# Kernel optimization log

Measured on AMD Instinct MI355X. Metric: run time of the kernel, lower is better.

## Reference

```python
import jax, jax.numpy as jnp
import numpy as np


def axisangle2mat(p):
    # p: [N, 6] = (rotation vector rx,ry,rz, translation tx,ty,tz) -> [N, 3, 4]
    v = p[:, :3]
    t = p[:, 3:]
    theta = jnp.sqrt(jnp.sum(v * v, axis=-1) + 1e-12)  # [N]
    k = v / theta[:, None]
    kx, ky, kz = k[:, 0], k[:, 1], k[:, 2]
    zero = jnp.zeros_like(kx)
    K = jnp.stack([
        jnp.stack([zero, -kz, ky], -1),
        jnp.stack([kz, zero, -kx], -1),
        jnp.stack([-ky, kx, zero], -1),
    ], -2)  # [N,3,3]
    I = jnp.eye(3, dtype=p.dtype)
    s = jnp.sin(theta)[:, None, None]
    c = (1.0 - jnp.cos(theta))[:, None, None]
    R = I + s * K + c * jnp.matmul(K, K)
    return jnp.concatenate([R, t[:, :, None]], axis=-1)  # [N,3,4]


def grid_sample_3d(vol, grid):
    # vol: [D,H,W]; grid: [...,3] with last dim (x,y,z) in [-1,1].
    # Replicates F.grid_sample(mode='bilinear', padding_mode='zeros', align_corners=False).
    D, H, W = vol.shape
    ix = ((grid[..., 0] + 1.0) * W - 1.0) * 0.5
    iy = ((grid[..., 1] + 1.0) * H - 1.0) * 0.5
    iz = ((grid[..., 2] + 1.0) * D - 1.0) * 0.5
    x0 = jnp.floor(ix); y0 = jnp.floor(iy); z0 = jnp.floor(iz)
    fx = ix - x0; fy = iy - y0; fz = iz - z0
    vol_flat = vol.reshape(-1)
    out = jnp.zeros(grid.shape[:-1], vol.dtype)
    for dz in (0, 1):
        for dy in (0, 1):
            for dx in (0, 1):
                xc = x0 + dx; yc = y0 + dy; zc = z0 + dz
                wgt = ((fx if dx else 1.0 - fx) * (fy if dy else 1.0 - fy) * (fz if dz else 1.0 - fz))
                valid = ((xc >= 0) & (xc < W) & (yc >= 0) & (yc < H) & (zc >= 0) & (zc < D))
                xi = jnp.clip(xc, 0, W - 1).astype(jnp.int32)
                yi = jnp.clip(yc, 0, H - 1).astype(jnp.int32)
                zi = jnp.clip(zc, 0, D - 1).astype(jnp.int32)
                v = vol_flat[(zi * H + yi) * W + xi]
                out = out + jnp.where(valid, v * wgt, 0.0)
    return out


def setup_inputs() -> dict:
    key = jax.random.key(0)
    ks = jax.random.split(key, 8)
    B, n, D, H, W = 4096, 2048, 256, 256, 256
    x = jax.random.normal(ks[0], (1, 1, D, H, W), dtype=jnp.float32)
    # voxel-space sample points inside the volume
    sampleGrid = jax.random.uniform(ks[1], (B, 3), dtype=jnp.float32) * jnp.array([W - 1, H - 1, D - 1], jnp.float32)
    ax = jnp.concatenate([
        jax.random.normal(ks[2], (B, 1, 3), dtype=jnp.float32) * 0.1,   # small rotations
        jax.random.normal(ks[3], (B, 1, 3), dtype=jnp.float32) * 5.0,   # translations (voxels)
    ], axis=-1)
    low = jax.random.uniform(ks[4], (B, 1, 3), dtype=jnp.float32) * 2.0
    ext = jax.random.uniform(ks[5], (B, 1, 3), dtype=jnp.float32) * 4.0 + 1.0
    bound = jnp.concatenate([low, low + ext], axis=1)  # [B,2,3], bound[:,1] > bound[:,0]
    A = jax.random.normal(ks[6], (B, 3, 3), dtype=jnp.float32) * 0.3
    InvCovScaled = jnp.einsum('bij,bkj->bik', A, A) + 0.5 * jnp.eye(3, dtype=jnp.float32)  # SPD
    xyz_psf = jax.random.normal(ks[7], (B, n, 3), dtype=jnp.float32)
    psf_sigma = jnp.ones((1,), jnp.float32)  # unused in forward (as in the original)
    return dict(x=x, sampleGrid=sampleGrid, ax=ax, bound=bound,
                InvCovScaled=InvCovScaled, psf_sigma=psf_sigma, xyz_psf=xyz_psf)


def reference(x, sampleGrid, ax, bound, InvCovScaled, psf_sigma, xyz_psf):
    # x: [1,1,D,H,W]; sampleGrid: [B,3]; ax: [B,1,6]; bound: [B,2,3];
    # InvCovScaled: [B,3,3]; xyz_psf: [B,n,3] (the torch.randn draw, made explicit)
    W = x.shape[-1]; H = x.shape[-2]; D = x.shape[-3]
    size = (W, H, D)  # matches torch: size = [x.shape[-1], x.shape[-2], x.shape[-3]]
    scaled_xyz_psf = 2.0 * jax.nn.sigmoid(xyz_psf) - 1.0                      # [B,n,3]
    half = (bound[:, 1, :] - bound[:, 0, :]) * 0.5                            # [B,3]
    bound_psf = scaled_xyz_psf * half[:, None]                                # [B,n,3]
    mat = axisangle2mat(ax.reshape(-1, 6)).reshape(ax.shape[:-1] + (3, 4))    # [B,1,3,4]
    R = mat[:, 0, :, :3]                                                      # [B,3,3]
    T = mat[:, 0, :, 3]                                                       # [B,3]
    # trans_first=True: R @ (p + T)
    mat_sampleGrid = jnp.einsum('bij,bj->bi', R, sampleGrid + T)[:, None]     # [B,1,3]
    psf_sampleGrid = mat_sampleGrid + bound_psf                               # [B,n,3]
    norm = jnp.array([size[0] - 1, size[1] - 1, size[2] - 1], psf_sampleGrid.dtype)
    grid = 2.0 * (psf_sampleGrid / norm - 0.5)
    psf_x = grid_sample_3d(x[0, 0], grid)                                     # [B,n]
    # Mahalanobis-style weights: exp(-0.5 * c^T InvCov c)
    q = jnp.einsum('bni,bij,bnj->bn', bound_psf, InvCovScaled, bound_psf)
    w = jnp.exp(-0.5 * q)                                                     # [B,n]
    y = jnp.sum(psf_x * w, axis=-1) / jnp.sum(w, axis=-1)                     # [B]
    return y
```

## Files before the change

### kernel.cpp

```cpp
#include <hip/hip_runtime.h>
#include <hip/hip_fp16.h>
#include <math.h>

constexpr int NT   = 256;
constexpr int WPB  = 4;
constexpr int DIMV = 256;
constexpr int RS   = 8;
constexpr int QROW = 9;
constexpr int QSLICE = RS * QROW;

__device__ __forceinline__ float rflf(float x) {
    return __uint_as_float(__builtin_amdgcn_readfirstlane(__float_as_uint(x)));
}
__device__ __forceinline__ float fexp2(float x) {
#if __has_builtin(__builtin_amdgcn_exp2f)
    return __builtin_amdgcn_exp2f(x);
#else
    return __expf(x * 0.6931471805599453f);
#endif
}
__device__ __forceinline__ float ffract(float x) {
#if __has_builtin(__builtin_amdgcn_fractf)
    return __builtin_amdgcn_fractf(x);
#else
    return x - floorf(x);
#endif
}
__device__ __forceinline__ unsigned pk16(float a, float b) {
    __half2 h = __float22half2_rn(make_float2(a, b));
    return __builtin_bit_cast(unsigned, h);
}
__device__ __forceinline__ __half2 u2h(unsigned u) {
    return __builtin_bit_cast(__half2, u);
}

__global__ __launch_bounds__(NT, 4) void psf_sample_kernel(
    const float* __restrict__ vol,
    const float* __restrict__ sampleGrid,
    const float* __restrict__ ax,
    const float* __restrict__ bound,
    const float* __restrict__ invcov,
    const float* __restrict__ xyz,
    float* __restrict__ out,
    int n, int B)
{
    const int tid  = threadIdx.x;
    const int wid  = tid >> 6;
    const int lane = tid & 63;
    const int b    = blockIdx.x * WPB + wid;
    const bool valid = b < B;

    __shared__ uint4 s_q[WPB][RS * QSLICE];

    const float LOG2E = 1.4426950408889634f;
    float cix = 0, ciy = 0, ciz = 0, hx = 0, hy = 0, hz = 0, addrC = 0;
    float Bxx = 0, Byy = 0, Bzz = 0, Bxy = 0, Bxz = 0, Byz = 0;
    bool fast = false;

    if (valid) {
        const float v0 = ax[b*6+0], v1 = ax[b*6+1], v2 = ax[b*6+2];
        const float t0 = ax[b*6+3], t1 = ax[b*6+4], t2 = ax[b*6+5];
        const float theta = sqrtf(v0*v0 + v1*v1 + v2*v2 + 1e-12f);
        const float inv = 1.0f / theta;
        const float kx = v0*inv, ky = v1*inv, kz = v2*inv;
        const float sn = __sinf(theta);
        const float cn = 1.0f - __cosf(theta);
        const float R00 = 1.0f - cn*(ky*ky + kz*kz);
        const float R01 = -sn*kz + cn*kx*ky;
        const float R02 =  sn*ky + cn*kx*kz;
        const float R10 =  sn*kz + cn*kx*ky;
        const float R11 = 1.0f - cn*(kx*kx + kz*kz);
        const float R12 = -sn*kx + cn*ky*kz;
        const float R20 = -sn*ky + cn*kx*kz;
        const float R21 =  sn*kx + cn*ky*kz;
        const float R22 = 1.0f - cn*(kx*kx + ky*ky);
        const float g0 = sampleGrid[b*3+0] + t0;
        const float g1 = sampleGrid[b*3+1] + t1;
        const float g2 = sampleGrid[b*3+2] + t2;
        const float ms0 = R00*g0 + R01*g1 + R02*g2;
        const float ms1 = R10*g0 + R11*g1 + R12*g2;
        const float ms2 = R20*g0 + R21*g1 + R22*g2;
        const float h0 = (bound[b*6+3] - bound[b*6+0]) * 0.5f;
        const float h1 = (bound[b*6+4] - bound[b*6+1]) * 0.5f;
        const float h2 = (bound[b*6+5] - bound[b*6+2]) * 0.5f;
        const float M00 = invcov[b*9+0], M01 = invcov[b*9+1], M02 = invcov[b*9+2];
        const float M11 = invcov[b*9+4], M12 = invcov[b*9+5], M22 = invcov[b*9+8];

        Bxx = rflf(-0.5f * M00 * h0 * h0 * LOG2E);
        Byy = rflf(-0.5f * M11 * h1 * h1 * LOG2E);
        Bzz = rflf(-0.5f * M22 * h2 * h2 * LOG2E);
        Bxy = rflf(-M01 * h0 * h1 * LOG2E);
        Bxz = rflf(-M02 * h0 * h2 * LOG2E);
        Byz = rflf(-M12 * h1 * h2 * LOG2E);

        const float kk = 256.0f / 255.0f;
        cix = rflf(fmaf(ms0, kk, -0.5f));
        ciy = rflf(fmaf(ms1, kk, -0.5f));
        ciz = rflf(fmaf(ms2, kk, -0.5f));
        hx  = rflf(h0 * kk);
        hy  = rflf(h1 * kk);
        hz  = rflf(h2 * kk);

        const int bx = __builtin_amdgcn_readfirstlane((int)floorf(cix - hx - 1e-3f));
        const int by = __builtin_amdgcn_readfirstlane((int)floorf(ciy - hy - 1e-3f));
        const int bz = __builtin_amdgcn_readfirstlane((int)floorf(ciz - hz - 1e-3f));
        addrC = rflf((float)(bz * QSLICE + by * QROW + bx));
        fast = (hx <= 2.9f) && (hy <= 2.9f) && (hz <= 2.9f);

        if (fast) {
            const int lx = lane & 7, ly = lane >> 3;
            float pv = 0.0f, pdx = 0.0f, pdy = 0.0f, pdxy = 0.0f;
            #pragma unroll
            for (int p = 0; p < RS; ++p) {
                const int gx = bx + lx, gy = by + ly, gz = bz + p;
                float v = 0.0f;
                if ((unsigned)gx < (unsigned)DIMV && (unsigned)gy < (unsigned)DIMV &&
                    (unsigned)gz < (unsigned)DIMV)
                    v = vol[((size_t)gz * DIMV + gy) * DIMV + gx];
                const float v10 = __shfl(v, (lane + 1) & 63);
                const float v01 = __shfl(v, (lane + 8) & 63);
                const float v11 = __shfl(v, (lane + 9) & 63);
                const float dx  = v10 - v;
                const float dy  = v01 - v;
                const float dxy = (v11 - v10) - dy;
                if (p > 0) {
                    s_q[wid][((p - 1) * RS + ly) * QROW + lx] =
                        make_uint4(pk16(pv, v), pk16(pdx, dx),
                                   pk16(pdy, dy), pk16(pdxy, dxy));
                }
                pv = v; pdx = dx; pdy = dy; pdxy = dxy;
            }
        }
    }
    __syncthreads();

    if (valid) {
        float sum_wx = 0.0f, sum_w = 0.0f;
        const uint4* __restrict__ sreg = s_q[wid];

        auto doSample = [&](float rx, float ry, float rz) {
            const float ex = fexp2(rx * -LOG2E);
            const float ey = fexp2(ry * -LOG2E);
            const float ez = fexp2(rz * -LOG2E);
            const float sx = (1.0f - ex) * __builtin_amdgcn_rcpf(1.0f + ex);
            const float sy = (1.0f - ey) * __builtin_amdgcn_rcpf(1.0f + ey);
            const float sz = (1.0f - ez) * __builtin_amdgcn_rcpf(1.0f + ez);

            const float ixf = fmaf(sx, hx, cix);
            const float iyf = fmaf(sy, hy, ciy);
            const float izf = fmaf(sz, hz, ciz);
            const float x0f = floorf(ixf), y0f = floorf(iyf), z0f = floorf(izf);
            const float fx = ffract(ixf), fy = ffract(iyf), fz = ffract(izf);

            float val;
            if (fast) {
                const float ef = fmaf(z0f, (float)QSLICE,
                                 fmaf(y0f, (float)QROW, x0f - addrC));
                const int e = (int)ef;
                const uint4 q = sreg[e];
                const __half2 v01  = u2h(q.x);
                const __half2 dx01 = u2h(q.y);
                const __half2 dy01 = u2h(q.z);
                const __half2 dxy01= u2h(q.w);
                const __half2 fx2  = __float2half2_rn(fx);
                const __half2 fy2  = __float2half2_rn(fy);
                const __half2 fxy2 = __hmul2(fx2, fy2);
                const __half2 acc  = __hfma2(fxy2, dxy01,
                                     __hfma2(fy2, dy01,
                                     __hfma2(fx2, dx01, v01)));
                const float a0 = __low2float(acc);
                const float a1 = __high2float(acc);
                val = fmaf(fz, a1 - a0, a0);
            } else {
                const int x0 = (int)x0f, y0 = (int)y0f, z0 = (int)z0f;
                const int x1 = x0 + 1, y1 = y0 + 1, z1 = z0 + 1;
                const bool vx0 = (unsigned)x0 < (unsigned)DIMV;
                const bool vx1 = (unsigned)x1 < (unsigned)DIMV;
                const bool vy0 = (unsigned)y0 < (unsigned)DIMV;
                const bool vy1 = (unsigned)y1 < (unsigned)DIMV;
                const bool vz0 = (unsigned)z0 < (unsigned)DIMV;
                const bool vz1 = (unsigned)z1 < (unsigned)DIMV;
                const int cx0 = min(max(x0,0),DIMV-1), cx1 = min(max(x1,0),DIMV-1);
                const int cy0 = min(max(y0,0),DIMV-1), cy1 = min(max(y1,0),DIMV-1);
                const int cz0 = min(max(z0,0),DIMV-1), cz1 = min(max(z1,0),DIMV-1);
                const float wx0 = 1.0f-fx, wx1 = fx, wy0 = 1.0f-fy, wy1 = fy;
                const float wz0 = 1.0f-fz, wz1 = fz;
                const int r00 = (cz0*DIMV + cy0)*DIMV, r01 = (cz0*DIMV + cy1)*DIMV;
                const int r10 = (cz1*DIMV + cy0)*DIMV, r11 = (cz1*DIMV + cy1)*DIMV;
                val  = (vz0&&vy0&&vx0) ? vol[r00+cx0]*(wz0*wy0*wx0) : 0.0f;
                val += (vz0&&vy0&&vx1) ? vol[r00+cx1]*(wz0*wy0*wx1) : 0.0f;
                val += (vz0&&vy1&&vx0) ? vol[r01+cx0]*(wz0*wy1*wx0) : 0.0f;
                val += (vz0&&vy1&&vx1) ? vol[r01+cx1]*(wz0*wy1*wx1) : 0.0f;
                val += (vz1&&vy0&&vx0) ? vol[r10+cx0]*(wz1*wy0*wx0) : 0.0f;
                val += (vz1&&vy0&&vx1) ? vol[r10+cx1]*(wz1*wy0*wx1) : 0.0f;
                val += (vz1&&vy1&&vx0) ? vol[r11+cx0]*(wz1*wy1*wx0) : 0.0f;
                val += (vz1&&vy1&&vx1) ? vol[r11+cx1]*(wz1*wy1*wx1) : 0.0f;
            }

            const float i1 = fmaf(Bxx, sx, fmaf(Bxy, sy, Bxz * sz));
            const float i2 = fmaf(Byy, sy, Byz * sz);
            const float i3 = Bzz * sz;
            const float f  = fmaf(sx, i1, fmaf(sy, i2, sz * i3));
            const float w = fexp2(f);
            sum_w  += w;
            sum_wx = fmaf(w, val, sum_wx);
        };

        const int ng = n >> 2;
        const float4* __restrict__ xb4 =
            reinterpret_cast<const float4*>(xyz + (size_t)b * n * 3);
        for (int g = lane; g < ng; g += 64) {
            const float4 q0 = xb4[g*3 + 0];
            const float4 q1 = xb4[g*3 + 1];
            const float4 q2 = xb4[g*3 + 2];
            doSample(q0.x, q0.y, q0.z);
            doSample(q0.w, q1.x, q1.y);
            doSample(q1.z, q1.w, q2.x);
            doSample(q2.y, q2.z, q2.w);
        }
        const float* __restrict__ xb = xyz + (size_t)b * n * 3;
        for (int i = (ng << 2) + lane; i < n; i += 64)
            doSample(xb[i*3+0], xb[i*3+1], xb[i*3+2]);

        #pragma unroll
        for (int off = 32; off > 0; off >>= 1) {
            sum_wx += __shfl_down(sum_wx, off);
            sum_w  += __shfl_down(sum_w,  off);
        }
        if (lane == 0) out[b] = sum_wx / sum_w;
    }
}

extern "C" void kernel_launch(void* const* d_in, const int* in_sizes, int n_in,
                              void* d_out, int out_size, void* d_ws, size_t ws_size,
                              hipStream_t stream) {
    const float* vol        = (const float*)d_in[0];
    const float* sampleGrid = (const float*)d_in[1];
    const float* ax         = (const float*)d_in[2];
    const float* bound      = (const float*)d_in[3];
    const float* invcov     = (const float*)d_in[4];
    const float* xyz        = (const float*)d_in[6];
    float* out              = (float*)d_out;

    const int B = in_sizes[1] / 3;
    const int n = in_sizes[6] / (B * 3);

    const int grid = (B + WPB - 1) / WPB;
    psf_sample_kernel<<<grid, NT, 0, stream>>>(vol, sampleGrid, ax, bound,
                                               invcov, xyz, out, n, B);
}
```

Measured before the change: 28.36 us.

## Double-buffer xyz offsets into LDS via async global_load_lds and shrink blocks

Streams each wave's per-sample offset data into a double-buffered LDS staging area using async global-to-LDS loads. The next chunk is prefetched while the current one is processed, so load latency overlaps the sampling arithmetic. Blocks shrink to 2 waves with no minimum-occupancy hint, and the block-wide barrier after the LDS table build is removed because each wave only uses its own slice. Risks include the manual vmcnt wait interacting with other outstanding loads, a missing LDS visibility barrier within the wave, and higher LDS use per block reducing occupancy.

```diff
diff --git a/kernel.cpp b/kernel.cpp
--- a/kernel.cpp
+++ b/kernel.cpp
@@ -2,12 +2,14 @@
 #include <hip/hip_fp16.h>
 #include <math.h>
 
-constexpr int NT   = 256;
-constexpr int WPB  = 4;
+constexpr int NT   = 128;
+constexpr int WPB  = 2;
 constexpr int DIMV = 256;
 constexpr int RS   = 8;
 constexpr int QROW = 9;
 constexpr int QSLICE = RS * QROW;
+constexpr int CH   = 256;
+constexpr int CHV  = CH * 3 / 4;
 
 __device__ __forceinline__ float rflf(float x) {
     return __uint_as_float(__builtin_amdgcn_readfirstlane(__float_as_uint(x)));
@@ -34,7 +36,7 @@
     return __builtin_bit_cast(__half2, u);
 }
 
-__global__ __launch_bounds__(NT, 4) void psf_sample_kernel(
+__global__ __launch_bounds__(NT) void psf_sample_kernel(
     const float* __restrict__ vol,
     const float* __restrict__ sampleGrid,
     const float* __restrict__ ax,
@@ -50,7 +52,8 @@
     const int b    = blockIdx.x * WPB + wid;
     const bool valid = b < B;
 
-    __shared__ uint4 s_q[WPB][RS * QSLICE];
+    __shared__ uint4  s_q[WPB][RS * QSLICE];
+    __shared__ float4 s_xyz[WPB][2][CHV];
 
     const float LOG2E = 1.4426950408889634f;
     float cix = 0, ciy = 0, ciz = 0, hx = 0, hy = 0, hz = 0, addrC = 0;
@@ -131,10 +134,7 @@
                 pv = v; pdx = dx; pdy = dy; pdxy = dxy;
             }
         }
-    }
-    __syncthreads();
-
-    if (valid) {
+
         float sum_wx = 0.0f, sum_w = 0.0f;
         const uint4* __restrict__ sreg = s_q[wid];
 
@@ -206,20 +206,37 @@
             sum_wx = fmaf(w, val, sum_wx);
         };
 
-        const int ng = n >> 2;
-        const float4* __restrict__ xb4 =
-            reinterpret_cast<const float4*>(xyz + (size_t)b * n * 3);
-        for (int g = lane; g < ng; g += 64) {
-            const float4 q0 = xb4[g*3 + 0];
-            const float4 q1 = xb4[g*3 + 1];
-            const float4 q2 = xb4[g*3 + 2];
-            doSample(q0.x, q0.y, q0.z);
-            doSample(q0.w, q1.x, q1.y);
-            doSample(q1.z, q1.w, q2.x);
-            doSample(q2.y, q2.z, q2.w);
+        const float* __restrict__ xb = xyz + (size_t)b * n * 3;
+        const int nch = n / CH;
+
+        auto issue = [&](int c, int bufi) {
+            const float* gp = xb + c * (CH * 3) + lane * 4;
+            #pragma unroll
+            for (int k = 0; k < 3; ++k) {
+                __builtin_amdgcn_global_load_lds(
+                    (const __attribute__((address_space(1))) float*)(gp + k * 256),
+                    (__attribute__((address_space(3))) float*)
+                        (&s_xyz[wid][bufi][k * 64]),
+                    16, 0, 0);
+            }
+        };
+
+        if (nch > 0) {
+            issue(0, 0);
+            for (int c = 0; c < nch; ++c) {
+                const int cur = c & 1;
+                issue(c + 1 < nch ? c + 1 : c, cur ^ 1);
+                asm volatile("s_waitcnt vmcnt(3)" ::: "memory");
+                const float4 q0 = s_xyz[wid][cur][lane * 3 + 0];
+                const float4 q1 = s_xyz[wid][cur][lane * 3 + 1];
+                const float4 q2 = s_xyz[wid][cur][lane * 3 + 2];
+                doSample(q0.x, q0.y, q0.z);
+                doSample(q0.w, q1.x, q1.y);
+                doSample(q1.z, q1.w, q2.x);
+                doSample(q2.y, q2.z, q2.w);
+            }
         }
-        const float* __restrict__ xb = xyz + (size_t)b * n * 3;
-        for (int i = (ng << 2) + lane; i < n; i += 64)
+        for (int i = nch * CH + lane; i < n; i += 64)
             doSample(xb[i*3+0], xb[i*3+1], xb[i*3+2]);
 
         #pragma unroll
```

New measurement: 37.67 us. +32.8%, slower.
